# Kernel tuning notes

Measured on AMD Instinct MI355X. Metric: run time of the kernel, lower is better.

The kernel has to match this reference:

```python
import jax, jax.numpy as jnp
import numpy as np

B, C, H, W_IMG = 16, 3, 384, 384
P = 16
G = H // P                 # 24
NPATCH = G * G             # 576
SEQ = NPATCH + 1           # 577 (with cls token)
D, FF, NH, NL = 768, 3072, 12, 12
NCLS = 1000
K = int(0.5 * NPATCH)
HD = D // NH
EPS = 1e-6


def _ln(x, g, b):
    mu = jnp.mean(x, axis=-1, keepdims=True)
    var = jnp.mean((x - mu) ** 2, axis=-1, keepdims=True)
    return (x - mu) * jax.lax.rsqrt(var + EPS) * g + b


def setup_inputs() -> dict:
    key = jax.random.key(0)
    ks = jax.random.split(key, 12)
    s = 0.02
    return {
        "x": jax.random.normal(ks[0], (B, C, H, W_IMG), jnp.float32),
        "patch_w": jax.random.normal(ks[1], (D, C, P, P), jnp.float32) * s,
        "patch_b": jnp.zeros((D,), jnp.float32),
        "cls_tok": jax.random.normal(ks[2], (1, 1, D), jnp.float32) * s,
        "pos_emb": jax.random.normal(ks[3], (1, SEQ, D), jnp.float32) * s,
        "ln1_g": jnp.ones((NL, D), jnp.float32),
        "ln1_b": jnp.zeros((NL, D), jnp.float32),
        "Wqkv": jax.random.normal(ks[4], (NL, D, 3 * D), jnp.float32) * s,
        "bqkv": jnp.zeros((NL, 3 * D), jnp.float32),
        "Wo": jax.random.normal(ks[5], (NL, D, D), jnp.float32) * s,
        "bo": jnp.zeros((NL, D), jnp.float32),
        "ln2_g": jnp.ones((NL, D), jnp.float32),
        "ln2_b": jnp.zeros((NL, D), jnp.float32),
        "W1": jax.random.normal(ks[6], (NL, D, FF), jnp.float32) * s,
        "b1": jnp.zeros((NL, FF), jnp.float32),
        "W2": jax.random.normal(ks[7], (NL, FF, D), jnp.float32) * s,
        "b2": jnp.zeros((NL, D), jnp.float32),
        "lnf_g": jnp.ones((D,), jnp.float32),
        "lnf_b": jnp.zeros((D,), jnp.float32),
        "fc_w": jax.random.normal(ks[8], (D, NCLS), jnp.float32) * s,
        "fc_b": jnp.zeros((NCLS,), jnp.float32),
    }


def reference(x, patch_w, patch_b, cls_tok, pos_emb, ln1_g, ln1_b, Wqkv, bqkv,
              Wo, bo, ln2_g, ln2_b, W1, b1, W2, b2, lnf_g, lnf_b, fc_w, fc_b):
    b = x.shape[0]
    # patch embedding: strided conv -> (b, D, G, G) -> (b, NPATCH, D)
    patches = jax.lax.conv_general_dilated(
        x, patch_w, window_strides=(P, P), padding="VALID",
        dimension_numbers=("NCHW", "OIHW", "NCHW")) + patch_b[None, :, None, None]
    tok = patches.reshape(b, D, NPATCH).transpose(0, 2, 1)
    tok = jnp.concatenate([jnp.broadcast_to(cls_tok, (b, 1, D)), tok], axis=1)
    tok = tok + pos_emb  # seq matches original_seq_len, no resize

    # saliency = avg-pool of raw first input channel (net_G output is unused in the source)
    pooled = x[:, 0].reshape(b, G, P, G, P).mean(axis=(2, 4)).reshape(b, NPATCH)
    _, idx = jax.lax.top_k(jnp.abs(pooled), K)          # (b, K)
    spatial = tok[:, 1:, :]
    sel = jnp.take_along_axis(spatial, idx[:, :, None], axis=1)  # (b, K, D)
    h = jnp.concatenate([tok[:, :1, :], sel], axis=1)   # (b, K+1, D)
    S = h.shape[1]

    scale = 1.0 / np.sqrt(HD)
    for i in range(NL):
        y = _ln(h, ln1_g[i], ln1_b[i])
        qkv = y @ Wqkv[i] + bqkv[i]
        q, k_, v = jnp.split(qkv, 3, axis=-1)
        q = q.reshape(b, S, NH, HD)
        k_ = k_.reshape(b, S, NH, HD)
        v = v.reshape(b, S, NH, HD)
        att = jnp.einsum("bqhd,bkhd->bhqk", q, k_) * scale
        att = jax.nn.softmax(att, axis=-1)
        o = jnp.einsum("bhqk,bkhd->bqhd", att, v).reshape(b, S, D)
        h = h + (o @ Wo[i] + bo[i])
        y = _ln(h, ln2_g[i], ln2_b[i])
        h = h + (jax.nn.gelu(y @ W1[i] + b1[i], approximate=False) @ W2[i] + b2[i])

    cls_out = _ln(h, lnf_g, lnf_b)[:, 0]   # pool_type='tok'
    return cls_out @ fc_w + fc_b


if __name__ == "__main__":
    out = reference(**setup_inputs())
    print(out.shape)
```

## Files before the change

kernel.cpp:

```cpp
#include <hip/hip_runtime.h>
#include <hip/hip_bf16.h>
#include <math.h>

#define BB 16
#define SS 289
#define DD 768
#define FFD 3072
#define NHD 12
#define NLAY 12
#define KSEL 288
#define NPATCH 576

typedef short bf16x8 __attribute__((ext_vector_type(8)));
typedef short bf16x4 __attribute__((ext_vector_type(4)));
typedef float f32x4 __attribute__((ext_vector_type(4)));

typedef __attribute__((address_space(3))) void lds_t;
typedef __attribute__((address_space(1))) const void glb_t;

__device__ __forceinline__ void gload16(const void* g, void* l) {
    __builtin_amdgcn_global_load_lds((glb_t*)g, (lds_t*)l, 16, 0, 0);
}

__device__ __forceinline__ bf16x8 ds_read128(unsigned addr) {
    bf16x8 r;
    asm volatile("ds_read_b128 %0, %1" : "=v"(r) : "v"(addr));
    return r;
}

__device__ __forceinline__ float gelu_f(float v) {
    return 0.5f * v * (1.0f + erff(v * 0.70710678118654752f));
}

__device__ __forceinline__ void store_val(float* p, float v) { *p = v; }
__device__ __forceinline__ void store_val(__hip_bfloat16* p, float v) { *p = __float2bfloat16(v); }

__global__ __launch_bounds__(256) void pool_kernel(const float* __restrict__ x,
                                                   float* __restrict__ pooled) {
    int bp = blockIdx.x;
    int b = bp / NPATCH, p = bp - b * NPATCH;
    int gi = p / 24, gj = p - gi * 24;
    int tid = threadIdx.x;
    int pi = tid >> 4, pj = tid & 15;
    float v = x[((size_t)(b * 3) * 384 + gi * 16 + pi) * 384 + gj * 16 + pj];
    #pragma unroll
    for (int o = 32; o > 0; o >>= 1) v += __shfl_down(v, o);
    __shared__ float red[4];
    if ((tid & 63) == 0) red[tid >> 6] = v;
    __syncthreads();
    if (tid == 0) pooled[bp] = (red[0] + red[1] + red[2] + red[3]) * (1.0f / 256.0f);
}

__global__ __launch_bounds__(576) void topk_kernel(const float* __restrict__ pooled,
                                                   int* __restrict__ idxsel) {
    __shared__ float a[NPATCH];
    int b = blockIdx.x, tid = threadIdx.x;
    a[tid] = fabsf(pooled[b * NPATCH + tid]);
    __syncthreads();
    float mine = a[tid];
    int rank = 0;
    for (int j = 0; j < NPATCH; ++j) {
        float aj = a[j];
        rank += (aj > mine) || (aj == mine && j < tid);
    }
    if (rank < KSEL) idxsel[b * KSEL + rank] = tid;
}

__global__ __launch_bounds__(256) void convert_bf16(const float* __restrict__ in,
                                                    __hip_bfloat16* __restrict__ out,
                                                    int n) {
    int i = blockIdx.x * 256 + threadIdx.x;
    if (i < n) out[i] = __float2bfloat16(in[i]);
}

__global__ __launch_bounds__(256) void convert_layer(const float* __restrict__ wqkv,
                                                     const float* __restrict__ wo,
                                                     const float* __restrict__ w1,
                                                     const float* __restrict__ w2,
                                                     __hip_bfloat16* __restrict__ oqkv,
                                                     __hip_bfloat16* __restrict__ owo,
                                                     __hip_bfloat16* __restrict__ ow1,
                                                     __hip_bfloat16* __restrict__ ow2) {
    __shared__ float tb[32][33];
    int bid = blockIdx.x;
    const float* W; __hip_bfloat16* O; int K, N, tile;
    if (bid < 1728)      { W = wqkv; O = oqkv; K = 768;  N = 2304; tile = bid; }
    else if (bid < 2304) { W = wo;   O = owo;  K = 768;  N = 768;  tile = bid - 1728; }
    else if (bid < 4608) { W = w1;   O = ow1;  K = 768;  N = 3072; tile = bid - 2304; }
    else                 { W = w2;   O = ow2;  K = 3072; N = 768;  tile = bid - 4608; }
    int ntx = N >> 5;
    int n0 = (tile % ntx) << 5, k0 = (tile / ntx) << 5;
    int t = threadIdx.x;
    int r = t >> 3, c = (t & 7) << 2;
    float4 v = *(const float4*)&W[(size_t)(k0 + r) * N + n0 + c];
    tb[r][c] = v.x; tb[r][c + 1] = v.y; tb[r][c + 2] = v.z; tb[r][c + 3] = v.w;
    __syncthreads();
    int n = t >> 3, k = (t & 7) << 2;
    __hip_bfloat16* dst = &O[(size_t)(n0 + n) * K + k0 + k];
    #pragma unroll
    for (int j = 0; j < 4; ++j) dst[j] = __float2bfloat16(tb[k + j][n]);
}

__global__ __launch_bounds__(256) void im2col_kernel(const float* __restrict__ x,
                                                     const int* __restrict__ idxsel,
                                                     __hip_bfloat16* __restrict__ col) {
    int t = blockIdx.x;
    int b = t / KSEL, r = t - b * KSEL;
    int p = idxsel[b * KSEL + r];
    int gi = p / 24, gj = p - gi * 24;
    int tid = threadIdx.x;
    int pi = tid >> 4, pj = tid & 15;
    __hip_bfloat16* crow = col + (size_t)t * 768;
    #pragma unroll
    for (int c = 0; c < 3; ++c)
        crow[c * 256 + tid] = __float2bfloat16(
            x[((size_t)(b * 3 + c) * 384 + gi * 16 + pi) * 384 + gj * 16 + pj]);
}

__global__ __launch_bounds__(256) void assemble_tokens(const float* __restrict__ temp,
                                                       const float* __restrict__ cls_tok,
                                                       const float* __restrict__ pos_emb,
                                                       const int* __restrict__ idxsel,
                                                       float* __restrict__ h) {
    int row = blockIdx.x;
    int b = row / SS, s = row - b * SS;
    int tid = threadIdx.x;
    float* hrow = h + (size_t)row * DD;
    if (s == 0) {
        #pragma unroll
        for (int c = 0; c < 3; ++c) {
            int j = c * 256 + tid;
            hrow[j] = cls_tok[j] + pos_emb[j];
        }
    } else {
        int r = s - 1;
        int p = idxsel[b * KSEL + r];
        const float* trow = temp + (size_t)(b * KSEL + r) * DD;
        const float* pe = pos_emb + (size_t)(1 + p) * DD;
        #pragma unroll
        for (int c = 0; c < 3; ++c) {
            int j = c * 256 + tid;
            hrow[j] = trow[j] + pe[j];
        }
    }
}

template <typename T>
__global__ __launch_bounds__(256) void ln_kernel(const float* __restrict__ in,
                                                 T* __restrict__ out,
                                                 const float* __restrict__ g,
                                                 const float* __restrict__ be,
                                                 size_t in_stride) {
    int row = blockIdx.x;
    const float* r = in + (size_t)row * in_stride;
    T* w = out + (size_t)row * DD;
    int tid = threadIdx.x;
    float v0 = r[tid], v1 = r[256 + tid], v2 = r[512 + tid];
    float s = v0 + v1 + v2;
    #pragma unroll
    for (int o = 32; o > 0; o >>= 1) s += __shfl_down(s, o);
    __shared__ float red[4];
    if ((tid & 63) == 0) red[tid >> 6] = s;
    __syncthreads();
    float mu = (red[0] + red[1] + red[2] + red[3]) * (1.0f / 768.0f);
    float d0 = v0 - mu, d1 = v1 - mu, d2 = v2 - mu;
    float q = d0 * d0 + d1 * d1 + d2 * d2;
    #pragma unroll
    for (int o = 32; o > 0; o >>= 1) q += __shfl_down(q, o);
    __syncthreads();
    if ((tid & 63) == 0) red[tid >> 6] = q;
    __syncthreads();
    float var = (red[0] + red[1] + red[2] + red[3]) * (1.0f / 768.0f);
    float rs = rsqrtf(var + 1e-6f);
    store_val(&w[tid],       d0 * rs * g[tid]       + be[tid]);
    store_val(&w[256 + tid], d1 * rs * g[256 + tid] + be[256 + tid]);
    store_val(&w[512 + tid], d2 * rs * g[512 + tid] + be[512 + tid]);
}

template <typename OUT_T, int ACT, int RES, int SPLITK>
__global__ __launch_bounds__(512) void gemm_bf16(const __hip_bfloat16* __restrict__ A,
                                                 const __hip_bfloat16* __restrict__ BT,
                                                 OUT_T* __restrict__ C,
                                                 const float* __restrict__ bias,
                                                 const float* __restrict__ res,
                                                 float* __restrict__ part,
                                                 int M, int N, int K) {
    __shared__ __hip_bfloat16 smA[3][128 * 32];
    __shared__ __hip_bfloat16 smB[3][256 * 32];
    const int t = threadIdx.x;
    const int lane = t & 63, wid = t >> 6;
    const int wr = wid >> 2, wc = wid & 3;
    const int l15 = lane & 15, l4 = lane >> 4;

    const int gx = gridDim.x;
    const int nwg = gx * gridDim.y;
    const int orig = blockIdx.y * gx + blockIdx.x;
    const int q8 = nwg >> 3, r8 = nwg & 7;
    const int xcd = orig & 7, linb = orig >> 3;
    const int swz = (xcd < r8 ? xcd * (q8 + 1) : r8 * (q8 + 1) + (xcd - r8) * q8) + linb;
    const int m0 = (swz / gx) << 7;
    const int n0 = (swz - (swz / gx) * gx) << 8;

    const int Ksub = K / SPLITK;
    const int kz0 = blockIdx.z * Ksub;

    int ra[4], rb[4];
    #pragma unroll
    for (int f = 0; f < 4; ++f) {
        int ml = wr * 64 + f * 16 + l15;
        ra[f] = ml * 64 + ((l4 ^ ((ml >> 1) & 3)) << 4);
        int nl = wc * 64 + f * 16 + l15;
        rb[f] = nl * 64 + ((l4 ^ ((nl >> 1) & 3)) << 4);
    }

    size_t aoff, boff[2];
    {
        int mA = t >> 2;
        int kcA = (t & 3) ^ ((mA >> 1) & 3);
        int gmA = m0 + mA; if (gmA > M - 1) gmA = M - 1;
        aoff = (size_t)gmA * K + kz0 + kcA * 8;
        #pragma unroll
        for (int it = 0; it < 2; ++it) {
            int s = it * 512 + t;
            int mB = s >> 2;
            int kc = (s & 3) ^ ((mB >> 1) & 3);
            boff[it] = (size_t)(n0 + mB) * K + kz0 + kc * 8;
        }
    }
    const int wb = wid << 10;
    const unsigned ldsA0 = (unsigned)(size_t)(lds_t*)&smA[0][0];
    const unsigned ldsB0 = (unsigned)(size_t)(lds_t*)&smB[0][0];

    auto STAGE = [&](int kt, int buf) {
        int k0e = kt << 5;
        gload16(A + aoff + k0e,     (char*)(&smA[buf][0]) + wb);
        gload16(BT + boff[0] + k0e, (char*)(&smB[buf][0]) + wb);
        gload16(BT + boff[1] + k0e, (char*)(&smB[buf][0]) + 8192 + wb);
    };

    f32x4 acc[4][4];
    #pragma unroll
    for (int i = 0; i < 4; ++i)
        #pragma unroll
        for (int j = 0; j < 4; ++j) acc[i][j] = (f32x4){0.f, 0.f, 0.f, 0.f};

    const int nt = Ksub >> 5;
    STAGE(0, 0); STAGE(1, 1);
    int cur = 0, stb = 2;
    for (int kt = 0; kt < nt; ++kt) {
        if (kt + 1 < nt) asm volatile("s_waitcnt vmcnt(3)" ::: "memory");
        else             asm volatile("s_waitcnt vmcnt(0)" ::: "memory");
        asm volatile("s_barrier" ::: "memory");
        if (kt + 2 < nt) STAGE(kt + 2, stb);
        const unsigned sa = ldsA0 + cur * 8192u;
        const unsigned sb = ldsB0 + cur * 16384u;
        bf16x8 af[4], bf[4];
        #pragma unroll
        for (int f = 0; f < 4; ++f) {
            af[f] = ds_read128(sa + ra[f]);
            bf[f] = ds_read128(sb + rb[f]);
        }
        asm volatile("s_waitcnt lgkmcnt(0)" ::: "memory");
        __builtin_amdgcn_sched_barrier(0);
        #pragma unroll
        for (int i = 0; i < 4; ++i)
            #pragma unroll
            for (int j = 0; j < 4; ++j)
                acc[i][j] = __builtin_amdgcn_mfma_f32_16x16x32_bf16(af[i], bf[j], acc[i][j], 0, 0, 0);
        cur = cur == 2 ? 0 : cur + 1;
        stb = stb == 2 ? 0 : stb + 1;
    }

    if (SPLITK == 1) {
        #pragma unroll
        for (int i = 0; i < 4; ++i) {
            int gmb = m0 + wr * 64 + i * 16 + l4 * 4;
            #pragma unroll
            for (int j = 0; j < 4; ++j) {
                int gn = n0 + wc * 64 + j * 16 + l15;
                float bv = bias ? bias[gn] : 0.f;
                #pragma unroll
                for (int r = 0; r < 4; ++r) {
                    int gm = gmb + r;
                    if (gm < M) {
                        float v = acc[i][j][r] + bv;
                        if (ACT) v = gelu_f(v);
                        if (RES) v += res[(size_t)gm * N + gn];
                        store_val(&C[(size_t)gm * N + gn], v);
                    }
                }
            }
        }
    } else {
        float* pz = part + (size_t)blockIdx.z * M * N;
        #pragma unroll
        for (int i = 0; i < 4; ++i) {
            int gmb = m0 + wr * 64 + i * 16 + l4 * 4;
            #pragma unroll
            for (int j = 0; j < 4; ++j) {
                int gn = n0 + wc * 64 + j * 16 + l15;
                #pragma unroll
                for (int r = 0; r < 4; ++r) {
                    int gm = gmb + r;
                    if (gm < M) pz[(size_t)gm * N + gn] = acc[i][j][r];
                }
            }
        }
    }
}

template <int NPART>
__global__ __launch_bounds__(256) void combine_res(const float* __restrict__ part,
                                                   const float* __restrict__ bias,
                                                   float* __restrict__ h,
                                                   int MN, int N) {
    int i = (blockIdx.x * 256 + threadIdx.x) * 4;
    if (i >= MN) return;
    float4 v = *(const float4*)&part[i];
    #pragma unroll
    for (int z = 1; z < NPART; ++z) {
        float4 p = *(const float4*)&part[(size_t)z * MN + i];
        v.x += p.x; v.y += p.y; v.z += p.z; v.w += p.w;
    }
    int n = i % N;
    float4 bv = *(const float4*)&bias[n];
    float4 hv = *(const float4*)&h[i];
    v.x += bv.x + hv.x; v.y += bv.y + hv.y; v.z += bv.z + hv.z; v.w += bv.w + hv.w;
    *(float4*)&h[i] = v;
}

__global__ __launch_bounds__(256) void head_gemm(const float* __restrict__ yf,
                                                 const float* __restrict__ fc_w,
                                                 const float* __restrict__ fc_b,
                                                 float* __restrict__ out) {
    __shared__ float ylds[4 * 768];
    const int tid = threadIdx.x;
    const int mh = blockIdx.y * 4;
    for (int i = tid; i < 4 * 768; i += 256) ylds[i] = yf[(size_t)(mh + (i >> 9) * 0 + i / 768) * 768 + i % 768];
    __syncthreads();
    const int n = blockIdx.x * 256 + tid;
    if (n >= 1000) return;
    float acc0 = 0.f, acc1 = 0.f, acc2 = 0.f, acc3 = 0.f;
    for (int k = 0; k < 768; ++k) {
        float w = fc_w[(size_t)k * 1000 + n];
        acc0 = fmaf(ylds[k], w, acc0);
        acc1 = fmaf(ylds[768 + k], w, acc1);
        acc2 = fmaf(ylds[1536 + k], w, acc2);
        acc3 = fmaf(ylds[2304 + k], w, acc3);
    }
    float b = fc_b[n];
    out[(size_t)(mh + 0) * 1000 + n] = acc0 + b;
    out[(size_t)(mh + 1) * 1000 + n] = acc1 + b;
    out[(size_t)(mh + 2) * 1000 + n] = acc2 + b;
    out[(size_t)(mh + 3) * 1000 + n] = acc3 + b;
}

__global__ __launch_bounds__(64) void attn_fused(const __hip_bfloat16* __restrict__ qkv,
                                                 __hip_bfloat16* __restrict__ o) {
    __shared__ __hip_bfloat16 p_lds[32][40];
    __shared__ __hip_bfloat16 v_lds[32][68];
    const int qt = blockIdx.x, bh = blockIdx.y;
    const int b = bh / NHD, hd = bh - b * NHD;
    const int lane = threadIdx.x;
    const int l15 = lane & 15, l4 = lane >> 4;
    const size_t tb = (size_t)b * SS;
    const int hc = hd * 64;

    bf16x8 aq[2][2];
    #pragma unroll
    for (int qi = 0; qi < 2; ++qi) {
        int qr = qt * 32 + qi * 16 + l15;
        if (qr >= SS) qr = SS - 1;
        const __hip_bfloat16* qrow = qkv + (tb + qr) * 2304 + hc;
        #pragma unroll
        for (int kd = 0; kd < 2; ++kd)
            aq[qi][kd] = *(const bf16x8*)(qrow + kd * 32 + l4 * 8);
    }

    float m_run[2][4], l_run[2][4];
    f32x4 oa[2][4];
    #pragma unroll
    for (int qi = 0; qi < 2; ++qi)
        #pragma unroll
        for (int r = 0; r < 4; ++r) { m_run[qi][r] = -1e30f; l_run[qi][r] = 0.f; }
    #pragma unroll
    for (int qi = 0; qi < 2; ++qi)
        #pragma unroll
        for (int dt = 0; dt < 4; ++dt) oa[qi][dt] = (f32x4){0.f, 0.f, 0.f, 0.f};

    for (int kt = 0; kt < 10; ++kt) {
        const int kbase = kt * 32;
        bf16x4 vreg[8];
        #pragma unroll
        for (int it = 0; it < 8; ++it) {
            int vr = kbase + it * 4 + l4;
            if (vr >= SS) vr = SS - 1;
            vreg[it] = *(const bf16x4*)(qkv + (tb + vr) * 2304 + 1536 + hc + l15 * 4);
        }
        bf16x8 bk[2][2];
        #pragma unroll
        for (int ki = 0; ki < 2; ++ki) {
            int kr = kbase + ki * 16 + l15;
            if (kr >= SS) kr = SS - 1;
            const __hip_bfloat16* krow = qkv + (tb + kr) * 2304 + 768 + hc;
            #pragma unroll
            for (int kd = 0; kd < 2; ++kd)
                bk[ki][kd] = *(const bf16x8*)(krow + kd * 32 + l4 * 8);
        }
        f32x4 s[2][2];
        #pragma unroll
        for (int qi = 0; qi < 2; ++qi)
            #pragma unroll
            for (int ki = 0; ki < 2; ++ki) {
                f32x4 a = (f32x4){0.f, 0.f, 0.f, 0.f};
                #pragma unroll
                for (int kd = 0; kd < 2; ++kd)
                    a = __builtin_amdgcn_mfma_f32_16x16x32_bf16(aq[qi][kd], bk[ki][kd], a, 0, 0, 0);
                s[qi][ki] = a;
            }
        #pragma unroll
        for (int ki = 0; ki < 2; ++ki) {
            bool valid = (kbase + ki * 16 + l15) < SS;
            #pragma unroll
            for (int qi = 0; qi < 2; ++qi)
                #pragma unroll
                for (int r = 0; r < 4; ++r)
                    s[qi][ki][r] = valid ? s[qi][ki][r] * 0.125f : -1e30f;
        }
        float p[2][2][4];
        #pragma unroll
        for (int qi = 0; qi < 2; ++qi) {
            float tm[4];
            #pragma unroll
            for (int r = 0; r < 4; ++r) tm[r] = fmaxf(s[qi][0][r], s[qi][1][r]);
            #pragma unroll
            for (int sh = 1; sh < 16; sh <<= 1)
                #pragma unroll
                for (int r = 0; r < 4; ++r) tm[r] = fmaxf(tm[r], __shfl_xor(tm[r], sh));
            float rs[4];
            #pragma unroll
            for (int r = 0; r < 4; ++r) {
                float mn = fmaxf(m_run[qi][r], tm[r]);
                float corr = __expf(m_run[qi][r] - mn);
                m_run[qi][r] = mn;
                float p0 = __expf(s[qi][0][r] - mn);
                float p1 = __expf(s[qi][1][r] - mn);
                p[qi][0][r] = p0; p[qi][1][r] = p1;
                rs[r] = p0 + p1;
                l_run[qi][r] *= corr;
                #pragma unroll
                for (int dt = 0; dt < 4; ++dt) oa[qi][dt][r] *= corr;
            }
            #pragma unroll
            for (int sh = 1; sh < 16; sh <<= 1)
                #pragma unroll
                for (int r = 0; r < 4; ++r) rs[r] += __shfl_xor(rs[r], sh);
            #pragma unroll
            for (int r = 0; r < 4; ++r) l_run[qi][r] += rs[r];
        }
        #pragma unroll
        for (int qi = 0; qi < 2; ++qi)
            #pragma unroll
            for (int ki = 0; ki < 2; ++ki)
                #pragma unroll
                for (int r = 0; r < 4; ++r)
                    p_lds[qi * 16 + l4 * 4 + r][ki * 16 + l15] = __float2bfloat16(p[qi][ki][r]);
        #pragma unroll
        for (int it = 0; it < 8; ++it)
            *(bf16x4*)&v_lds[it * 4 + l4][l15 * 4] = vreg[it];
        __syncthreads();
        bf16x8 pa[2];
        #pragma unroll
        for (int qi = 0; qi < 2; ++qi)
            pa[qi] = *(const bf16x8*)&p_lds[qi * 16 + l15][l4 * 8];
        bf16x8 vb[4];
        #pragma unroll
        for (int dt = 0; dt < 4; ++dt) {
            bf16x8 v;
            #pragma unroll
            for (int j = 0; j < 8; ++j)
                v[j] = *(const short*)&v_lds[l4 * 8 + j][dt * 16 + l15];
            vb[dt] = v;
        }
        #pragma unroll
        for (int qi = 0; qi < 2; ++qi)
            #pragma unroll
            for (int dt = 0; dt < 4; ++dt)
                oa[qi][dt] = __builtin_amdgcn_mfma_f32_16x16x32_bf16(pa[qi], vb[dt], oa[qi][dt], 0, 0, 0);
        __syncthreads();
    }
    #pragma unroll
    for (int qi = 0; qi < 2; ++qi)
        #pragma unroll
        for (int r = 0; r < 4; ++r) {
            int q = qt * 32 + qi * 16 + l4 * 4 + r;
            if (q < SS) {
                float inv = 1.0f / l_run[qi][r];
                __hip_bfloat16* orow = o + (tb + q) * 768 + hc;
                #pragma unroll
                for (int dt = 0; dt < 4; ++dt)
                    orow[dt * 16 + l15] = __float2bfloat16(oa[qi][dt][r] * inv);
            }
        }
}

static const size_t OFF_POOLED = 0;
static const size_t OFF_IDX    = 10240;
static const size_t OFF_H      = 16384;
static const size_t OFF_YB     = 3567616;
static const size_t OFF_OB     = 5343232;
static const size_t OFF_QKVB   = 7118848;
static const size_t OFF_WBUF   = 12445696;
static const size_t OFF_PWB    = 15984640;
static const size_t OFF_YF     = 16279552;
static const size_t OFF_BIG    = 16291840;
static const size_t OFF_PART   = 23394304;

extern "C" void kernel_launch(void* const* d_in, const int* in_sizes, int n_in,
                              void* d_out, int out_size, void* d_ws, size_t ws_size,
                              hipStream_t stream) {
    const float* x       = (const float*)d_in[0];
    const float* patch_w = (const float*)d_in[1];
    const float* patch_b = (const float*)d_in[2];
    const float* cls_tok = (const float*)d_in[3];
    const float* pos_emb = (const float*)d_in[4];
    const float* ln1_g   = (const float*)d_in[5];
    const float* ln1_b   = (const float*)d_in[6];
    const float* Wqkv    = (const float*)d_in[7];
    const float* bqkv    = (const float*)d_in[8];
    const float* Wo      = (const float*)d_in[9];
    const float* bo      = (const float*)d_in[10];
    const float* ln2_g   = (const float*)d_in[11];
    const float* ln2_b   = (const float*)d_in[12];
    const float* W1      = (const float*)d_in[13];
    const float* b1      = (const float*)d_in[14];
    const float* W2      = (const float*)d_in[15];
    const float* b2      = (const float*)d_in[16];
    const float* lnf_g   = (const float*)d_in[17];
    const float* lnf_b   = (const float*)d_in[18];
    const float* fc_w    = (const float*)d_in[19];
    const float* fc_b    = (const float*)d_in[20];
    float* out = (float*)d_out;
    float* ws  = (float*)d_ws;

    float*          pooled = ws + OFF_POOLED;
    int*            idxsel = (int*)(ws + OFF_IDX);
    float*          h      = ws + OFF_H;
    __hip_bfloat16* yb     = (__hip_bfloat16*)(ws + OFF_YB);
    __hip_bfloat16* ob     = (__hip_bfloat16*)(ws + OFF_OB);
    __hip_bfloat16* qkvb   = (__hip_bfloat16*)(ws + OFF_QKVB);
    __hip_bfloat16* wbuf   = (__hip_bfloat16*)(ws + OFF_WBUF);
    __hip_bfloat16* pwb    = (__hip_bfloat16*)(ws + OFF_PWB);
    float*          yf     = ws + OFF_YF;
    float*          big    = ws + OFF_BIG;
    float*          part   = ws + OFF_PART;
    __hip_bfloat16* col    = (__hip_bfloat16*)big;
    float*          temp   = big + 1769472;
    __hip_bfloat16* hidden = (__hip_bfloat16*)big;

    __hip_bfloat16* wqkvT = wbuf;
    __hip_bfloat16* woT   = wbuf + 1769472;
    __hip_bfloat16* w1T   = wbuf + 2359296;
    __hip_bfloat16* w2T   = wbuf + 4718592;

    const int M = BB * SS;
    const int MG = 37;
    const int MN = M * DD;

    pool_kernel<<<BB * NPATCH, 256, 0, stream>>>(x, pooled);
    topk_kernel<<<BB, 576, 0, stream>>>(pooled, idxsel);
    convert_bf16<<<(589824 + 255) / 256, 256, 0, stream>>>(patch_w, pwb, 589824);
    im2col_kernel<<<BB * KSEL, 256, 0, stream>>>(x, idxsel, col);
    gemm_bf16<float, 0, 0, 1><<<dim3(3, 36), 512, 0, stream>>>(
        col, pwb, temp, patch_b, nullptr, nullptr, 4608, DD, DD);
    assemble_tokens<<<BB * SS, 256, 0, stream>>>(temp, cls_tok, pos_emb, idxsel, h);

    for (int i = 0; i < NLAY; ++i) {
        convert_layer<<<6912, 256, 0, stream>>>(Wqkv + (size_t)i * DD * 3 * DD,
                                                Wo + (size_t)i * DD * DD,
                                                W1 + (size_t)i * DD * FFD,
                                                W2 + (size_t)i * FFD * DD,
                                                wqkvT, woT, w1T, w2T);

        ln_kernel<__hip_bfloat16><<<M, 256, 0, stream>>>(h, yb, ln1_g + i * DD, ln1_b + i * DD, DD);
        gemm_bf16<__hip_bfloat16, 0, 0, 1><<<dim3(9, MG), 512, 0, stream>>>(
            yb, wqkvT, qkvb, bqkv + (size_t)i * 3 * DD, nullptr, nullptr, M, 3 * DD, DD);
        attn_fused<<<dim3(10, BB * NHD), 64, 0, stream>>>(qkvb, ob);
        gemm_bf16<float, 0, 0, 2><<<dim3(3, MG, 2), 512, 0, stream>>>(
            ob, woT, (float*)nullptr, nullptr, nullptr, part, M, DD, DD);
        combine_res<2><<<(MN / 4 + 255) / 256, 256, 0, stream>>>(part, bo + (size_t)i * DD, h, MN, DD);
        ln_kernel<__hip_bfloat16><<<M, 256, 0, stream>>>(h, yb, ln2_g + i * DD, ln2_b + i * DD, DD);
        gemm_bf16<__hip_bfloat16, 1, 0, 1><<<dim3(12, MG), 512, 0, stream>>>(
            yb, w1T, hidden, b1 + (size_t)i * FFD, nullptr, nullptr, M, FFD, DD);
        gemm_bf16<float, 0, 0, 4><<<dim3(3, MG, 4), 512, 0, stream>>>(
            hidden, w2T, (float*)nullptr, nullptr, nullptr, part, M, DD, FFD);
        combine_res<4><<<(MN / 4 + 255) / 256, 256, 0, stream>>>(part, b2 + (size_t)i * DD, h, MN, DD);
    }

    ln_kernel<float><<<BB, 256, 0, stream>>>(h, yf, lnf_g, lnf_b, (size_t)SS * DD);
    head_gemm<<<dim3(4, 4), 256, 0, stream>>>(yf, fc_w, fc_b, out);
}
```

Baseline: 2.464 ms.

## Fuse split-K combine with residual and following LayerNorm; retile head GEMM

```diff
diff --git a/kernel.cpp b/kernel.cpp
--- a/kernel.cpp
+++ b/kernel.cpp
@@ -10,6 +10,7 @@
 #define NLAY 12
 #define KSEL 288
 #define NPATCH 576
+#define MNTOT 3551232
 
 typedef short bf16x8 __attribute__((ext_vector_type(8)));
 typedef short bf16x4 __attribute__((ext_vector_type(4)));
@@ -97,8 +98,10 @@
     __syncthreads();
     int n = t >> 3, k = (t & 7) << 2;
     __hip_bfloat16* dst = &O[(size_t)(n0 + n) * K + k0 + k];
-    #pragma unroll
-    for (int j = 0; j < 4; ++j) dst[j] = __float2bfloat16(tb[k + j][n]);
+    __hip_bfloat16 o4[4];
+    #pragma unroll
+    for (int j = 0; j < 4; ++j) o4[j] = __float2bfloat16(tb[k + j][n]);
+    *(bf16x4*)dst = *(const bf16x4*)o4;
 }
 
 __global__ __launch_bounds__(256) void im2col_kernel(const float* __restrict__ x,
@@ -329,30 +332,68 @@
     *(float4*)&h[i] = v;
 }
 
+template <int NPART>
+__global__ __launch_bounds__(256) void combine_ln(const float* __restrict__ part,
+                                                  const float* __restrict__ bias,
+                                                  float* __restrict__ h,
+                                                  const float* __restrict__ g,
+                                                  const float* __restrict__ be,
+                                                  __hip_bfloat16* __restrict__ out) {
+    int row = blockIdx.x, tid = threadIdx.x;
+    size_t base = (size_t)row * DD;
+    float a[3];
+    #pragma unroll
+    for (int k = 0; k < 3; ++k) {
+        int j = k * 256 + tid;
+        float s = part[base + j];
+        #pragma unroll
+        for (int z = 1; z < NPART; ++z) s += part[(size_t)z * MNTOT + base + j];
+        s += bias[j] + h[base + j];
+        h[base + j] = s;
+        a[k] = s;
+    }
+    float s = a[0] + a[1] + a[2];
+    #pragma unroll
+    for (int o = 32; o > 0; o >>= 1) s += __shfl_down(s, o);
+    __shared__ float red[4];
+    if ((tid & 63) == 0) red[tid >> 6] = s;
+    __syncthreads();
+    float mu = (red[0] + red[1] + red[2] + red[3]) * (1.0f / 768.0f);
+    float d0 = a[0] - mu, d1 = a[1] - mu, d2 = a[2] - mu;
+    float q = d0 * d0 + d1 * d1 + d2 * d2;
+    #pragma unroll
+    for (int o = 32; o > 0; o >>= 1) q += __shfl_down(q, o);
+    __syncthreads();
+    if ((tid & 63) == 0) red[tid >> 6] = q;
+    __syncthreads();
+    float var = (red[0] + red[1] + red[2] + red[3]) * (1.0f / 768.0f);
+    float rs = rsqrtf(var + 1e-6f);
+    out[base + tid]       = __float2bfloat16(d0 * rs * g[tid]       + be[tid]);
+    out[base + 256 + tid] = __float2bfloat16(d1 * rs * g[256 + tid] + be[256 + tid]);
+    out[base + 512 + tid] = __float2bfloat16(d2 * rs * g[512 + tid] + be[512 + tid]);
+}
+
 __global__ __launch_bounds__(256) void head_gemm(const float* __restrict__ yf,
                                                  const float* __restrict__ fc_w,
                                                  const float* __restrict__ fc_b,
                                                  float* __restrict__ out) {
-    __shared__ float ylds[4 * 768];
+    __shared__ float part[128];
     const int tid = threadIdx.x;
-    const int mh = blockIdx.y * 4;
-    for (int i = tid; i < 4 * 768; i += 256) ylds[i] = yf[(size_t)(mh + (i >> 9) * 0 + i / 768) * 768 + i % 768];
-    __syncthreads();
-    const int n = blockIdx.x * 256 + tid;
-    if (n >= 1000) return;
-    float acc0 = 0.f, acc1 = 0.f, acc2 = 0.f, acc3 = 0.f;
-    for (int k = 0; k < 768; ++k) {
-        float w = fc_w[(size_t)k * 1000 + n];
-        acc0 = fmaf(ylds[k], w, acc0);
-        acc1 = fmaf(ylds[768 + k], w, acc1);
-        acc2 = fmaf(ylds[1536 + k], w, acc2);
-        acc3 = fmaf(ylds[2304 + k], w, acc3);
-    }
-    float b = fc_b[n];
-    out[(size_t)(mh + 0) * 1000 + n] = acc0 + b;
-    out[(size_t)(mh + 1) * 1000 + n] = acc1 + b;
-    out[(size_t)(mh + 2) * 1000 + n] = acc2 + b;
-    out[(size_t)(mh + 3) * 1000 + n] = acc3 + b;
+    const int nl = tid & 127, kh = tid >> 7;
+    const int m = blockIdx.y;
+    const int n = blockIdx.x * 128 + nl;
+    float acc = 0.f;
+    if (n < 1000) {
+        const float* yr = yf + (size_t)m * 768 + kh * 384;
+        const float* wp = fc_w + (size_t)kh * 384 * 1000 + n;
+        #pragma unroll 4
+        for (int k = 0; k < 384; ++k)
+            acc = fmaf(yr[k], wp[(size_t)k * 1000], acc);
+    }
+    if (kh == 1) part[nl] = acc;
+    __syncthreads();
+    if (kh == 0 && n < 1000)
+        out[(size_t)m * 1000 + n] = acc + part[nl] + fc_b[n];
 }
 
 __global__ __launch_bounds__(64) void attn_fused(const __hip_bfloat16* __restrict__ qkv,
@@ -575,6 +616,8 @@
         col, pwb, temp, patch_b, nullptr, nullptr, 4608, DD, DD);
     assemble_tokens<<<BB * SS, 256, 0, stream>>>(temp, cls_tok, pos_emb, idxsel, h);
 
+    ln_kernel<__hip_bfloat16><<<M, 256, 0, stream>>>(h, yb, ln1_g, ln1_b, DD);
+
     for (int i = 0; i < NLAY; ++i) {
         convert_layer<<<6912, 256, 0, stream>>>(Wqkv + (size_t)i * DD * 3 * DD,
                                                 Wo + (size_t)i * DD * DD,
@@ -582,21 +625,26 @@
                                                 W2 + (size_t)i * FFD * DD,
                                                 wqkvT, woT, w1T, w2T);
 
-        ln_kernel<__hip_bfloat16><<<M, 256, 0, stream>>>(h, yb, ln1_g + i * DD, ln1_b + i * DD, DD);
         gemm_bf16<__hip_bfloat16, 0, 0, 1><<<dim3(9, MG), 512, 0, stream>>>(
             yb, wqkvT, qkvb, bqkv + (size_t)i * 3 * DD, nullptr, nullptr, M, 3 * DD, DD);
         attn_fused<<<dim3(10, BB * NHD), 64, 0, stream>>>(qkvb, ob);
         gemm_bf16<float, 0, 0, 2><<<dim3(3, MG, 2), 512, 0, stream>>>(
             ob, woT, (float*)nullptr, nullptr, nullptr, part, M, DD, DD);
-        combine_res<2><<<(MN / 4 + 255) / 256, 256, 0, stream>>>(part, bo + (size_t)i * DD, h, MN, DD);
-        ln_kernel<__hip_bfloat16><<<M, 256, 0, stream>>>(h, yb, ln2_g + i * DD, ln2_b + i * DD, DD);
+        combine_ln<2><<<M, 256, 0, stream>>>(part, bo + (size_t)i * DD, h,
+                                             ln2_g + (size_t)i * DD, ln2_b + (size_t)i * DD, yb);
         gemm_bf16<__hip_bfloat16, 1, 0, 1><<<dim3(12, MG), 512, 0, stream>>>(
             yb, w1T, hidden, b1 + (size_t)i * FFD, nullptr, nullptr, M, FFD, DD);
         gemm_bf16<float, 0, 0, 4><<<dim3(3, MG, 4), 512, 0, stream>>>(
             hidden, w2T, (float*)nullptr, nullptr, nullptr, part, M, DD, FFD);
-        combine_res<4><<<(MN / 4 + 255) / 256, 256, 0, stream>>>(part, b2 + (size_t)i * DD, h, MN, DD);
+        if (i + 1 < NLAY)
+            combine_ln<4><<<M, 256, 0, stream>>>(part, b2 + (size_t)i * DD, h,
+                                                 ln1_g + (size_t)(i + 1) * DD,
+                                                 ln1_b + (size_t)(i + 1) * DD, yb);
+        else
+            combine_res<4><<<(MN / 4 + 255) / 256, 256, 0, stream>>>(
+                part, b2 + (size_t)i * DD, h, MN, DD);
     }
 
     ln_kernel<float><<<BB, 256, 0, stream>>>(h, yf, lnf_g, lnf_b, (size_t)SS * DD);
-    head_gemm<<<dim3(4, 4), 256, 0, stream>>>(yf, fc_w, fc_b, out);
-}
+    head_gemm<<<dim3(8, 16), 256, 0, stream>>>(yf, fc_w, fc_b, out);
+}
```

After: 2.351 ms. 1.05x faster.
